# Kernel tuning notes

Hardware: AMD Instinct MI355X
Metric: run time of the kernel (lower is better)

## Reference

```python
import jax, jax.numpy as jnp
import numpy as np
from jax import lax

BN_EPS = 1e-5
DIST_EPS = 1e-8

def _three_nn_interpolate(xyz1, xyz2, points2):
    # squared pairwise distances: (B, N, S)
    d2 = (jnp.sum(xyz1 ** 2, -1)[:, :, None]
          + jnp.sum(xyz2 ** 2, -1)[:, None, :]
          - 2.0 * jnp.einsum('bnd,bsd->bns', xyz1, xyz2))
    neg_d, idx = lax.top_k(-d2, 3)            # 3 nearest -> (B, N, 3)
    dist = -neg_d
    recip = 1.0 / (dist + DIST_EPS)
    weight = recip / jnp.sum(recip, -1, keepdims=True)   # (B, N, 3)
    gathered = jax.vmap(lambda p, i: p[i])(points2, idx)  # (B, N, 3, C2)
    return jnp.einsum('bnkc,bnk->bnc', gathered, weight)

def _conv_bn_relu(x, w, g, b):
    # x: (B, N, Cin); 1x1 conv == matmul; BatchNorm1d over (B, N) per channel (training stats)
    y = jnp.einsum('bnc,oc->bno', x, w)
    mu = jnp.mean(y, axis=(0, 1))
    var = jnp.mean((y - mu) ** 2, axis=(0, 1))
    yn = (y - mu) * lax.rsqrt(var + BN_EPS)
    return jax.nn.relu(yn * g + b)

def setup_inputs() -> dict:
    key = jax.random.key(0)
    ks = jax.random.split(key, 6)
    B, N, S, C1, C2 = 16, 4096, 1024, 256, 256
    return {
        'xyz1': jax.random.normal(ks[0], (B, N, 3), jnp.float32),
        'xyz2': jax.random.normal(ks[1], (B, S, 3), jnp.float32),
        'points1': jax.random.normal(ks[2], (B, N, C1), jnp.float32),
        'points2': jax.random.normal(ks[3], (B, S, C2), jnp.float32),
        'w1': jax.random.normal(ks[4], (256, C1 + C2), jnp.float32) * 0.04,
        'g1': jnp.ones((256,), jnp.float32),
        'b1': jnp.zeros((256,), jnp.float32),
        'w2': jax.random.normal(ks[5], (256, 256), jnp.float32) * 0.06,
        'g2': jnp.ones((256,), jnp.float32),
        'b2': jnp.zeros((256,), jnp.float32),
    }

def reference(xyz1, xyz2, points1, points2, w1, g1, b1, w2, g2, b2):
    interp = _three_nn_interpolate(xyz1, xyz2, points2)    # (B, N, C2)
    feats = jnp.concatenate([points1, interp], axis=-1)    # (B, N, C1+C2)
    h = _conv_bn_relu(feats, w1, g1, b1)
    out = _conv_bn_relu(h, w2, g2, b2)
    return out                                              # (B, N, 256)
```

## Files before the change

### kernel.cpp

```cpp
#include <hip/hip_runtime.h>
#include <stdint.h>

typedef unsigned short ushort_t;
typedef __bf16 bf16x8 __attribute__((ext_vector_type(8)));
typedef float f32x4 __attribute__((ext_vector_type(4)));
typedef unsigned short ushort8 __attribute__((ext_vector_type(8)));
typedef unsigned short ushort4_t __attribute__((ext_vector_type(4)));

#define DEV static __device__ __forceinline__

DEV unsigned short f2bf(float f) {
    union { float f; unsigned int i; } v; v.f = f;
    unsigned int u = v.i;
    return (unsigned short)((u + 0x7fffu + ((u >> 16) & 1u)) >> 16);
}
DEV float bf2f(unsigned short u) {
    union { unsigned int i; float f; } v; v.i = ((unsigned int)u) << 16; return v.f;
}
DEV bf16x8 u2b(ushort8 u) { union { ushort8 u; bf16x8 b; } x; x.u = u; return x.b; }

__global__ __launch_bounds__(256) void cvt_kernel(
    const float* __restrict__ in, ushort_t* __restrict__ out, int n)
{
    int i = blockIdx.x * 256 + threadIdx.x;
    if (i < n) out[i] = f2bf(in[i]);
}

__global__ __launch_bounds__(256) void cvt4_kernel(
    const float* __restrict__ in, ushort_t* __restrict__ out)
{
    int i = (blockIdx.x * 256 + threadIdx.x) * 4;
    float4 v = *(const float4*)(in + i);
    ushort4_t o;
    o[0] = f2bf(v.x); o[1] = f2bf(v.y); o[2] = f2bf(v.z); o[3] = f2bf(v.w);
    *(ushort4_t*)(out + i) = o;
}

__global__ __launch_bounds__(256) void knn_kernel(
    const float* __restrict__ xyz1, const float* __restrict__ xyz2,
    int* __restrict__ idx_out, float* __restrict__ w_out)
{
    __shared__ float4 P[1024];
    __shared__ float mD[24][32];
    __shared__ int   mI[24][32];
    const int b = blockIdx.y;
    const int tid = threadIdx.x;
    for (int s = tid; s < 1024; s += 256) {
        const float* p = xyz2 + ((size_t)b * 1024 + s) * 3;
        float x = p[0], y = p[1], z = p[2];
        float pp = __fadd_rn(__fadd_rn(__fmul_rn(x, x), __fmul_rn(y, y)), __fmul_rn(z, z));
        P[s] = make_float4(x, y, z, pp);
    }
    __syncthreads();
    const int ql = tid & 31;
    const int chunk = tid >> 5;
    const int n = blockIdx.x * 32 + ql;
    const float* q = xyz1 + ((size_t)b * 4096 + n) * 3;
    float qx = q[0], qy = q[1], qz = q[2];
    float qq = __fadd_rn(__fadd_rn(__fmul_rn(qx, qx), __fmul_rn(qy, qy)), __fmul_rn(qz, qz));
    float d0 = 1e30f, d1 = 1e30f, d2 = 1e30f;
    int i0 = 0, i1 = 0, i2 = 0;
    const int s0 = chunk * 128;
#pragma unroll 4
    for (int s = s0; s < s0 + 128; ++s) {
        float4 p = P[s];
        float dot = __fadd_rn(__fadd_rn(__fmul_rn(qx, p.x), __fmul_rn(qy, p.y)), __fmul_rn(qz, p.z));
        float d = __fsub_rn(__fadd_rn(qq, p.w), __fmul_rn(2.0f, dot));
        if (d < d2) {
            if (d < d1) {
                d2 = d1; i2 = i1;
                if (d < d0) { d1 = d0; i1 = i0; d0 = d; i0 = s; }
                else        { d1 = d;  i1 = s; }
            } else { d2 = d; i2 = s; }
        }
    }
    mD[chunk * 3 + 0][ql] = d0; mI[chunk * 3 + 0][ql] = i0;
    mD[chunk * 3 + 1][ql] = d1; mI[chunk * 3 + 1][ql] = i1;
    mD[chunk * 3 + 2][ql] = d2; mI[chunk * 3 + 2][ql] = i2;
    __syncthreads();
    if (tid < 32) {
        float e0 = 1e30f, e1 = 1e30f, e2 = 1e30f;
        int j0 = 0, j1 = 0, j2 = 0;
#pragma unroll
        for (int c = 0; c < 24; ++c) {
            float d = mD[c][ql]; int i = mI[c][ql];
            if (d < e2) {
                if (d < e1) {
                    e2 = e1; j2 = j1;
                    if (d < e0) { e1 = e0; j1 = j0; e0 = d; j0 = i; }
                    else        { e1 = d;  j1 = i; }
                } else { e2 = d; j2 = i; }
            }
        }
        float r0 = 1.0f / (e0 + 1e-8f);
        float r1 = 1.0f / (e1 + 1e-8f);
        float r2 = 1.0f / (e2 + 1e-8f);
        float rs = __fadd_rn(__fadd_rn(r0, r1), r2);
        size_t o = ((size_t)b * 4096 + n) * 3;
        idx_out[o + 0] = j0; idx_out[o + 1] = j1; idx_out[o + 2] = j2;
        w_out[o + 0] = r0 / rs; w_out[o + 1] = r1 / rs; w_out[o + 2] = r2 / rs;
    }
}

__global__ __launch_bounds__(256) void interp_kernel(
    const ushort_t* __restrict__ p2b, const int* __restrict__ idx,
    const float* __restrict__ wgt, ushort_t* __restrict__ itp)
{
    const int t = blockIdx.x * 256 + threadIdx.x;
    const int q = t >> 3;
    const int cg = (t & 7) * 32;
    const size_t o = (size_t)q * 3;
    int i0 = idx[o], i1 = idx[o + 1], i2 = idx[o + 2];
    float w0 = wgt[o], w1 = wgt[o + 1], w2 = wgt[o + 2];
    const ushort_t* pb = p2b + (size_t)(q >> 12) * (1024 * 256);
    const ushort8* g0 = (const ushort8*)(pb + (size_t)i0 * 256 + cg);
    const ushort8* g1 = (const ushort8*)(pb + (size_t)i1 * 256 + cg);
    const ushort8* g2 = (const ushort8*)(pb + (size_t)i2 * 256 + cg);
    ushort8* dst = (ushort8*)(itp + (size_t)q * 256 + cg);
#pragma unroll
    for (int s = 0; s < 4; ++s) {
        ushort8 a = g0[s], b = g1[s], c = g2[s];
        ushort8 ov;
#pragma unroll
        for (int j = 0; j < 8; ++j) {
            float acc = __fmul_rn(w0, bf2f(a[j]));
            acc = fmaf(w1, bf2f(b[j]), acc);
            acc = fmaf(w2, bf2f(c[j]), acc);
            ov[j] = f2bf(acc);
        }
        dst[s] = ov;
    }
}

DEV void cvt8(const float4& u0, const float4& u1, ushort8& hv) {
    hv[0] = f2bf(u0.x); hv[1] = f2bf(u0.y); hv[2] = f2bf(u0.z); hv[3] = f2bf(u0.w);
    hv[4] = f2bf(u1.x); hv[5] = f2bf(u1.y); hv[6] = f2bf(u1.z); hv[7] = f2bf(u1.w);
}

__global__ __launch_bounds__(1024, 4) void gemm1_kernel(
    const float* __restrict__ p1, const ushort_t* __restrict__ itp,
    const ushort_t* __restrict__ w1b, ushort_t* __restrict__ y,
    float* __restrict__ sums, float* __restrict__ sqs)
{
    __shared__ __align__(16) char smem[133120];
    ushort_t* Bs = (ushort_t*)smem;
    const int tid = threadIdx.x;
    const int wave = tid >> 6, lane = tid & 63;
    const int frl = lane & 15, fq = lane >> 4;
    const int panel = blockIdx.x >> 1, nb = blockIdx.x & 1;
    const int m0 = panel * 256;

    {
        const int c = tid >> 3, qq = tid & 7;
        const ushort_t* src = w1b + (size_t)(nb * 128 + c) * 512;
        ushort_t* dst = Bs + c * 520;
#pragma unroll
        for (int s = 0; s < 8; ++s) {
            int off = qq * 8 + s * 64;
            *(ushort8*)(dst + off) = *(const ushort8*)(src + off);
        }
    }

    f32x4 acc[8];
#pragma unroll
    for (int j = 0; j < 8; ++j) acc[j] = f32x4{0.0f, 0.0f, 0.0f, 0.0f};

    __syncthreads();

    const int row0 = m0 + wave * 16 + frl;
    bf16x8 afb[2], bfb[2][8];

#define G1_LOADA(buf, kc) {                                                        \
    if ((kc) < 8) {                                                                \
        const float4* g = (const float4*)(p1 + (size_t)row0 * 256                  \
                                          + (kc) * 32 + fq * 8);                   \
        float4 u0 = g[0], u1 = g[1];                                               \
        ushort8 hv; cvt8(u0, u1, hv);                                              \
        buf = u2b(hv);                                                             \
    } else {                                                                       \
        buf = *(const bf16x8*)(itp + (size_t)row0 * 256                            \
                               + ((kc) - 8) * 32 + fq * 8);                        \
    } }
#define G1_LOADB(buf, kc) { _Pragma("unroll")                                      \
    for (int j = 0; j < 8; ++j)                                                    \
        buf[j] = *(const bf16x8*)(Bs + (j * 16 + frl) * 520 + (kc) * 32 + fq * 8); }

    G1_LOADA(afb[0], 0); G1_LOADB(bfb[0], 0);
#pragma unroll
    for (int kc = 0; kc < 16; ++kc) {
        const int cur = kc & 1, nxt = cur ^ 1;
        if (kc < 15) { G1_LOADA(afb[nxt], kc + 1); G1_LOADB(bfb[nxt], kc + 1); }
#pragma unroll
        for (int j = 0; j < 8; ++j)
            acc[j] = __builtin_amdgcn_mfma_f32_16x16x32_bf16(afb[cur], bfb[cur][j], acc[j], 0, 0, 0);
    }

    float ps[8], pq[8];
#pragma unroll
    for (int j = 0; j < 8; ++j) {
        const int colg = nb * 128 + j * 16 + frl;
        float s = 0.f, q = 0.f;
#pragma unroll
        for (int rr = 0; rr < 4; ++rr) {
            ushort_t hb = f2bf(acc[j][rr]);
            float v = bf2f(hb);
            y[(size_t)(m0 + wave * 16 + fq * 4 + rr) * 256 + colg] = hb;
            s += v; q = fmaf(v, v, q);
        }
        s += __shfl_xor(s, 16); s += __shfl_xor(s, 32);
        q += __shfl_xor(q, 16); q += __shfl_xor(q, 32);
        ps[j] = s; pq[j] = q;
    }
    __syncthreads();
    float* scrS = (float*)smem;
    float* scrQ = (float*)(smem + 8192);
    if (fq == 0) {
#pragma unroll
        for (int j = 0; j < 8; ++j) {
            scrS[wave * 128 + j * 16 + frl] = ps[j];
            scrQ[wave * 128 + j * 16 + frl] = pq[j];
        }
    }
    __syncthreads();
    if (tid < 128) {
        float s = 0.f, q = 0.f;
#pragma unroll
        for (int w = 0; w < 16; ++w) { s += scrS[w * 128 + tid]; q += scrQ[w * 128 + tid]; }
        atomicAdd(&sums[nb * 128 + tid], s);
        atomicAdd(&sqs[nb * 128 + tid], q);
    }
}

__global__ __launch_bounds__(512, 2) void gemm2_kernel(
    const ushort_t* __restrict__ y1, const ushort_t* __restrict__ w2b,
    const float* __restrict__ a1, const float* __restrict__ c1,
    ushort_t* __restrict__ y2, float* __restrict__ sums, float* __restrict__ sqs)
{
    __shared__ __align__(16) char smem[137216];
    ushort_t* As = (ushort_t*)smem;
    ushort_t* Bs = (ushort_t*)(smem + 67584);
    float* sAv = (float*)(smem + 135168);
    float* sCv = (float*)(smem + 136192);
    const int tid = threadIdx.x;
    const int wave = tid >> 6, lane = tid & 63;
    const int frl = lane & 15, fq = lane >> 4;
    const int panel = blockIdx.x >> 1, nb = blockIdx.x & 1;
    const int m0 = panel * 128;

    if (tid < 256) { sAv[tid] = a1[tid]; sCv[tid] = c1[tid]; }
    __syncthreads();

    {
        const int r = tid >> 2, qq = tid & 3;
        const ushort_t* srcA = y1 + (size_t)(m0 + r) * 256;
        ushort_t* dstA = As + r * 264;
        const ushort_t* srcB = w2b + (size_t)(nb * 128 + r) * 256;
        ushort_t* dstB = Bs + r * 264;
#pragma unroll
        for (int s = 0; s < 8; ++s) {
            int off = qq * 8 + s * 32;
            ushort8 raw = *(const ushort8*)(srcA + off);
            ushort8 hv;
#pragma unroll
            for (int e = 0; e < 8; ++e) {
                float v = bf2f(raw[e]);
                hv[e] = f2bf(fmaxf(fmaf(v, sAv[off + e], sCv[off + e]), 0.0f));
            }
            *(ushort8*)(dstA + off) = hv;
            *(ushort8*)(dstB + off) = *(const ushort8*)(srcB + off);
        }
    }

    f32x4 acc[2][4];
#pragma unroll
    for (int i = 0; i < 2; ++i)
#pragma unroll
        for (int j = 0; j < 4; ++j) acc[i][j] = f32x4{0.0f, 0.0f, 0.0f, 0.0f};

    __syncthreads();

    const int rg = (wave & 3) * 32, cg = (wave >> 2) * 64;
    bf16x8 afb[2][2], bfb[2][4];

#define G2_LOADA(buf, kc) { _Pragma("unroll")                                      \
    for (int i = 0; i < 2; ++i)                                                    \
        buf[i] = *(const bf16x8*)(As + (rg + i * 16 + frl) * 264 + (kc) * 32 + fq * 8); }
#define G2_LOADB(buf, kc) { _Pragma("unroll")                                      \
    for (int j = 0; j < 4; ++j)                                                    \
        buf[j] = *(const bf16x8*)(Bs + (cg + j * 16 + frl) * 264 + (kc) * 32 + fq * 8); }

    G2_LOADA(afb[0], 0); G2_LOADB(bfb[0], 0);
#pragma unroll
    for (int kc = 0; kc < 8; ++kc) {
        const int cur = kc & 1, nxt = cur ^ 1;
        if (kc < 7) { G2_LOADA(afb[nxt], kc + 1); G2_LOADB(bfb[nxt], kc + 1); }
#pragma unroll
        for (int i = 0; i < 2; ++i)
#pragma unroll
            for (int j = 0; j < 4; ++j)
                acc[i][j] = __builtin_amdgcn_mfma_f32_16x16x32_bf16(afb[cur][i], bfb[cur][j], acc[i][j], 0, 0, 0);
    }

    float ps[4], pq[4];
#pragma unroll
    for (int j = 0; j < 4; ++j) {
        const int colg = nb * 128 + cg + j * 16 + frl;
        float s = 0.f, q = 0.f;
#pragma unroll
        for (int i = 0; i < 2; ++i)
#pragma unroll
            for (int rr = 0; rr < 4; ++rr) {
                ushort_t hb = f2bf(acc[i][j][rr]);
                float v = bf2f(hb);
                y2[(size_t)(m0 + rg + i * 16 + fq * 4 + rr) * 256 + colg] = hb;
                s += v; q = fmaf(v, v, q);
            }
        s += __shfl_xor(s, 16); s += __shfl_xor(s, 32);
        q += __shfl_xor(q, 16); q += __shfl_xor(q, 32);
        ps[j] = s; pq[j] = q;
    }
    __syncthreads();
    float* scrS = (float*)smem;
    float* scrQ = (float*)(smem + 2048);
    if (fq == 0) {
#pragma unroll
        for (int j = 0; j < 4; ++j) {
            scrS[wave * 64 + j * 16 + frl] = ps[j];
            scrQ[wave * 64 + j * 16 + frl] = pq[j];
        }
    }
    __syncthreads();
    if (tid < 128) {
        const int g = tid >> 6, cw = tid & 63;
        float s = 0.f, q = 0.f;
#pragma unroll
        for (int k = 0; k < 4; ++k) {
            s += scrS[(g * 4 + k) * 64 + cw];
            q += scrQ[(g * 4 + k) * 64 + cw];
        }
        atomicAdd(&sums[nb * 128 + g * 64 + cw], s);
        atomicAdd(&sqs[nb * 128 + g * 64 + cw], q);
    }
}

__global__ __launch_bounds__(256) void finalize_kernel(
    const float* __restrict__ sums, const float* __restrict__ sqs,
    const float* __restrict__ g, const float* __restrict__ bias,
    float* __restrict__ a, float* __restrict__ c)
{
    const int ch = threadIdx.x;
    const float inv_n = 1.0f / 65536.0f;
    float mu = sums[ch] * inv_n;
    float var = fmaf(-mu, mu, sqs[ch] * inv_n);
    float is = 1.0f / sqrtf(var + 1e-5f);
    float aa = g[ch] * is;
    a[ch] = aa;
    c[ch] = fmaf(-mu, aa, bias[ch]);
}

__global__ __launch_bounds__(256) void apply_kernel(
    const ushort_t* __restrict__ y2, const float* __restrict__ a,
    const float* __restrict__ c, float* __restrict__ out)
{
    const size_t i = ((size_t)blockIdx.x * 256 + threadIdx.x) * 8;
    const int ch = (int)(i & 255);
    ushort8 raw = *(const ushort8*)(y2 + i);
    float4 o0, o1;
    const float4 a0 = *(const float4*)(a + ch), a1v = *(const float4*)(a + ch + 4);
    const float4 c0 = *(const float4*)(c + ch), c1v = *(const float4*)(c + ch + 4);
    o0.x = fmaxf(fmaf(bf2f(raw[0]), a0.x, c0.x), 0.0f);
    o0.y = fmaxf(fmaf(bf2f(raw[1]), a0.y, c0.y), 0.0f);
    o0.z = fmaxf(fmaf(bf2f(raw[2]), a0.z, c0.z), 0.0f);
    o0.w = fmaxf(fmaf(bf2f(raw[3]), a0.w, c0.w), 0.0f);
    o1.x = fmaxf(fmaf(bf2f(raw[4]), a1v.x, c1v.x), 0.0f);
    o1.y = fmaxf(fmaf(bf2f(raw[5]), a1v.y, c1v.y), 0.0f);
    o1.z = fmaxf(fmaf(bf2f(raw[6]), a1v.z, c1v.z), 0.0f);
    o1.w = fmaxf(fmaf(bf2f(raw[7]), a1v.w, c1v.w), 0.0f);
    *(float4*)(out + i) = o0;
    *(float4*)(out + i + 4) = o1;
}

extern "C" void kernel_launch(void* const* d_in, const int* in_sizes, int n_in,
                              void* d_out, int out_size, void* d_ws, size_t ws_size,
                              hipStream_t stream)
{
    const float* xyz1    = (const float*)d_in[0];
    const float* xyz2    = (const float*)d_in[1];
    const float* points1 = (const float*)d_in[2];
    const float* points2 = (const float*)d_in[3];
    const float* w1      = (const float*)d_in[4];
    const float* g1      = (const float*)d_in[5];
    const float* b1      = (const float*)d_in[6];
    const float* w2      = (const float*)d_in[7];
    const float* g2      = (const float*)d_in[8];
    const float* b2      = (const float*)d_in[9];
    float* out = (float*)d_out;

    char* ws = (char*)d_ws;
    float* sums1 = (float*)(ws + 0);
    float* sqs1  = (float*)(ws + 1024);
    float* a1    = (float*)(ws + 2048);
    float* c1    = (float*)(ws + 3072);
    float* sums2 = (float*)(ws + 4096);
    float* sqs2  = (float*)(ws + 5120);
    float* a2    = (float*)(ws + 6144);
    float* c2    = (float*)(ws + 7168);
    ushort_t* w1b = (ushort_t*)(ws + (64u << 10));
    ushort_t* w2b = (ushort_t*)(ws + (320u << 10));
    ushort_t* p2b = (ushort_t*)(ws + (1u << 20));
    int*   idx   = (int*)(ws + (10u << 20));
    float* wgt   = (float*)(ws + (11u << 20));
    ushort_t* itp = (ushort_t*)(ws + (12u << 20));
    ushort_t* y1  = (ushort_t*)(ws + (44u << 20));
    ushort_t* y2b = itp;

    hipMemsetAsync(ws, 0, 8192, stream);
    cvt_kernel<<<dim3(512), 256, 0, stream>>>(w1, w1b, 131072);
    cvt_kernel<<<dim3(256), 256, 0, stream>>>(w2, w2b, 65536);
    cvt4_kernel<<<dim3(4096), 256, 0, stream>>>(points2, p2b);
    knn_kernel<<<dim3(128, 16), 256, 0, stream>>>(xyz1, xyz2, idx, wgt);
    interp_kernel<<<dim3(2048), 256, 0, stream>>>(p2b, idx, wgt, itp);
    gemm1_kernel<<<dim3(512), 1024, 0, stream>>>(points1, itp, w1b, y1, sums1, sqs1);
    finalize_kernel<<<dim3(1), 256, 0, stream>>>(sums1, sqs1, g1, b1, a1, c1);
    gemm2_kernel<<<dim3(1024), 512, 0, stream>>>(y1, w2b, a1, c1, y2b, sums2, sqs2);
    finalize_kernel<<<dim3(1), 256, 0, stream>>>(sums2, sqs2, g2, b2, a2, c2);
    apply_kernel<<<dim3(8192), 256, 0, stream>>>(y2b, a2, c2, out);
}
```

Measured before the change: 285.1 us.

## Fuse interpolation into GEMM1, merge prep kernels, fold BN finalize into consumers

Removes the separate interpolation kernel: GEMM1 now gathers the three neighbour rows of bf16 points2 and blends them while loading its A operand. This avoids writing and re-reading the 32MB interpolated buffer. The three conversion kernels and the stats memset are merged into one prep kernel, and each BN finalize is recomputed per block inside gemm2 and apply, which cuts five launches. The cost is uncoalesced gather loads in GEMM1's inner loop and redundant per-block finalize math.

```diff
diff --git a/kernel.cpp b/kernel.cpp
--- a/kernel.cpp
+++ b/kernel.cpp
@@ -19,21 +19,30 @@
 }
 DEV bf16x8 u2b(ushort8 u) { union { ushort8 u; bf16x8 b; } x; x.u = u; return x.b; }
 
-__global__ __launch_bounds__(256) void cvt_kernel(
-    const float* __restrict__ in, ushort_t* __restrict__ out, int n)
-{
-    int i = blockIdx.x * 256 + threadIdx.x;
-    if (i < n) out[i] = f2bf(in[i]);
-}
-
-__global__ __launch_bounds__(256) void cvt4_kernel(
-    const float* __restrict__ in, ushort_t* __restrict__ out)
-{
-    int i = (blockIdx.x * 256 + threadIdx.x) * 4;
-    float4 v = *(const float4*)(in + i);
-    ushort4_t o;
-    o[0] = f2bf(v.x); o[1] = f2bf(v.y); o[2] = f2bf(v.z); o[3] = f2bf(v.w);
-    *(ushort4_t*)(out + i) = o;
+__global__ __launch_bounds__(256) void prep_kernel(
+    const float* __restrict__ w1, const float* __restrict__ w2,
+    const float* __restrict__ points2,
+    ushort_t* __restrict__ w1b, ushort_t* __restrict__ w2b,
+    ushort_t* __restrict__ p2b, float* __restrict__ stats)
+{
+    const int bx = blockIdx.x;
+    if (bx < 512) {
+        int i = bx * 256 + threadIdx.x;
+        w1b[i] = f2bf(w1[i]);
+    } else if (bx < 768) {
+        int i = (bx - 512) * 256 + threadIdx.x;
+        w2b[i] = f2bf(w2[i]);
+    } else if (bx < 4864) {
+        int i = ((bx - 768) * 256 + threadIdx.x) * 4;
+        float4 v = *(const float4*)(points2 + i);
+        ushort4_t o;
+        o[0] = f2bf(v.x); o[1] = f2bf(v.y); o[2] = f2bf(v.z); o[3] = f2bf(v.w);
+        *(ushort4_t*)(p2b + i) = o;
+    } else {
+        int i = threadIdx.x * 8;
+        *(float4*)(stats + i)     = make_float4(0.f, 0.f, 0.f, 0.f);
+        *(float4*)(stats + i + 4) = make_float4(0.f, 0.f, 0.f, 0.f);
+    }
 }
 
 __global__ __launch_bounds__(256) void knn_kernel(
@@ -102,43 +111,14 @@
     }
 }
 
-__global__ __launch_bounds__(256) void interp_kernel(
-    const ushort_t* __restrict__ p2b, const int* __restrict__ idx,
-    const float* __restrict__ wgt, ushort_t* __restrict__ itp)
-{
-    const int t = blockIdx.x * 256 + threadIdx.x;
-    const int q = t >> 3;
-    const int cg = (t & 7) * 32;
-    const size_t o = (size_t)q * 3;
-    int i0 = idx[o], i1 = idx[o + 1], i2 = idx[o + 2];
-    float w0 = wgt[o], w1 = wgt[o + 1], w2 = wgt[o + 2];
-    const ushort_t* pb = p2b + (size_t)(q >> 12) * (1024 * 256);
-    const ushort8* g0 = (const ushort8*)(pb + (size_t)i0 * 256 + cg);
-    const ushort8* g1 = (const ushort8*)(pb + (size_t)i1 * 256 + cg);
-    const ushort8* g2 = (const ushort8*)(pb + (size_t)i2 * 256 + cg);
-    ushort8* dst = (ushort8*)(itp + (size_t)q * 256 + cg);
-#pragma unroll
-    for (int s = 0; s < 4; ++s) {
-        ushort8 a = g0[s], b = g1[s], c = g2[s];
-        ushort8 ov;
-#pragma unroll
-        for (int j = 0; j < 8; ++j) {
-            float acc = __fmul_rn(w0, bf2f(a[j]));
-            acc = fmaf(w1, bf2f(b[j]), acc);
-            acc = fmaf(w2, bf2f(c[j]), acc);
-            ov[j] = f2bf(acc);
-        }
-        dst[s] = ov;
-    }
-}
-
 DEV void cvt8(const float4& u0, const float4& u1, ushort8& hv) {
     hv[0] = f2bf(u0.x); hv[1] = f2bf(u0.y); hv[2] = f2bf(u0.z); hv[3] = f2bf(u0.w);
     hv[4] = f2bf(u1.x); hv[5] = f2bf(u1.y); hv[6] = f2bf(u1.z); hv[7] = f2bf(u1.w);
 }
 
 __global__ __launch_bounds__(1024, 4) void gemm1_kernel(
-    const float* __restrict__ p1, const ushort_t* __restrict__ itp,
+    const float* __restrict__ p1, const ushort_t* __restrict__ p2b,
+    const int* __restrict__ idx, const float* __restrict__ wgt,
     const ushort_t* __restrict__ w1b, ushort_t* __restrict__ y,
     float* __restrict__ sums, float* __restrict__ sqs)
 {
@@ -165,9 +145,16 @@
 #pragma unroll
     for (int j = 0; j < 8; ++j) acc[j] = f32x4{0.0f, 0.0f, 0.0f, 0.0f};
 
-    __syncthreads();
-
     const int row0 = m0 + wave * 16 + frl;
+    const size_t io = (size_t)row0 * 3;
+    const float iw0 = wgt[io], iw1 = wgt[io + 1], iw2 = wgt[io + 2];
+    const ushort_t* pb = p2b + (size_t)(row0 >> 12) * (1024 * 256);
+    const ushort_t* gp0 = pb + (size_t)idx[io] * 256 + fq * 8;
+    const ushort_t* gp1 = pb + (size_t)idx[io + 1] * 256 + fq * 8;
+    const ushort_t* gp2 = pb + (size_t)idx[io + 2] * 256 + fq * 8;
+
+    __syncthreads();
+
     bf16x8 afb[2], bfb[2][8];
 
 #define G1_LOADA(buf, kc) {                                                        \
@@ -178,8 +165,18 @@
         ushort8 hv; cvt8(u0, u1, hv);                                              \
         buf = u2b(hv);                                                             \
     } else {                                                                       \
-        buf = *(const bf16x8*)(itp + (size_t)row0 * 256                            \
-                               + ((kc) - 8) * 32 + fq * 8);                        \
+        ushort8 ga = *(const ushort8*)(gp0 + ((kc) - 8) * 32);                     \
+        ushort8 gb = *(const ushort8*)(gp1 + ((kc) - 8) * 32);                     \
+        ushort8 gc = *(const ushort8*)(gp2 + ((kc) - 8) * 32);                     \
+        ushort8 hv;                                                                \
+        _Pragma("unroll")                                                          \
+        for (int e = 0; e < 8; ++e) {                                              \
+            float av = __fmul_rn(iw0, bf2f(ga[e]));                                \
+            av = fmaf(iw1, bf2f(gb[e]), av);                                       \
+            av = fmaf(iw2, bf2f(gc[e]), av);                                       \
+            hv[e] = f2bf(av);                                                      \
+        }                                                                          \
+        buf = u2b(hv);                                                             \
     } }
 #define G1_LOADB(buf, kc) { _Pragma("unroll")                                      \
     for (int j = 0; j < 8; ++j)                                                    \
@@ -233,7 +230,8 @@
 
 __global__ __launch_bounds__(512, 2) void gemm2_kernel(
     const ushort_t* __restrict__ y1, const ushort_t* __restrict__ w2b,
-    const float* __restrict__ a1, const float* __restrict__ c1,
+    const float* __restrict__ sums1, const float* __restrict__ sqs1,
+    const float* __restrict__ g1, const float* __restrict__ b1,
     ushort_t* __restrict__ y2, float* __restrict__ sums, float* __restrict__ sqs)
 {
     __shared__ __align__(16) char smem[137216];
@@ -247,7 +245,15 @@
     const int panel = blockIdx.x >> 1, nb = blockIdx.x & 1;
     const int m0 = panel * 128;
 
-    if (tid < 256) { sAv[tid] = a1[tid]; sCv[tid] = c1[tid]; }
+    if (tid < 256) {
+        const float inv_n = 1.0f / 65536.0f;
+        float mu = sums1[tid] * inv_n;
+        float var = fmaf(-mu, mu, sqs1[tid] * inv_n);
+        float is = 1.0f / sqrtf(var + 1e-5f);
+        float aa = g1[tid] * is;
+        sAv[tid] = aa;
+        sCv[tid] = fmaf(-mu, aa, b1[tid]);
+    }
     __syncthreads();
 
     {
@@ -343,31 +349,30 @@
     }
 }
 
-__global__ __launch_bounds__(256) void finalize_kernel(
-    const float* __restrict__ sums, const float* __restrict__ sqs,
-    const float* __restrict__ g, const float* __restrict__ bias,
-    float* __restrict__ a, float* __restrict__ c)
-{
-    const int ch = threadIdx.x;
-    const float inv_n = 1.0f / 65536.0f;
-    float mu = sums[ch] * inv_n;
-    float var = fmaf(-mu, mu, sqs[ch] * inv_n);
-    float is = 1.0f / sqrtf(var + 1e-5f);
-    float aa = g[ch] * is;
-    a[ch] = aa;
-    c[ch] = fmaf(-mu, aa, bias[ch]);
-}
-
 __global__ __launch_bounds__(256) void apply_kernel(
-    const ushort_t* __restrict__ y2, const float* __restrict__ a,
-    const float* __restrict__ c, float* __restrict__ out)
-{
+    const ushort_t* __restrict__ y2,
+    const float* __restrict__ sums2, const float* __restrict__ sqs2,
+    const float* __restrict__ g2, const float* __restrict__ b2,
+    float* __restrict__ out)
+{
+    __shared__ float sA[256], sC[256];
+    {
+        const int ch2 = threadIdx.x;
+        const float inv_n = 1.0f / 65536.0f;
+        float mu = sums2[ch2] * inv_n;
+        float var = fmaf(-mu, mu, sqs2[ch2] * inv_n);
+        float is = 1.0f / sqrtf(var + 1e-5f);
+        float aa = g2[ch2] * is;
+        sA[ch2] = aa;
+        sC[ch2] = fmaf(-mu, aa, b2[ch2]);
+    }
+    __syncthreads();
     const size_t i = ((size_t)blockIdx.x * 256 + threadIdx.x) * 8;
     const int ch = (int)(i & 255);
     ushort8 raw = *(const ushort8*)(y2 + i);
     float4 o0, o1;
-    const float4 a0 = *(const float4*)(a + ch), a1v = *(const float4*)(a + ch + 4);
-    const float4 c0 = *(const float4*)(c + ch), c1v = *(const float4*)(c + ch + 4);
+    const float4 a0 = *(const float4*)(sA + ch), a1v = *(const float4*)(sA + ch + 4);
+    const float4 c0 = *(const float4*)(sC + ch), c1v = *(const float4*)(sC + ch + 4);
     o0.x = fmaxf(fmaf(bf2f(raw[0]), a0.x, c0.x), 0.0f);
     o0.y = fmaxf(fmaf(bf2f(raw[1]), a0.y, c0.y), 0.0f);
     o0.z = fmaxf(fmaf(bf2f(raw[2]), a0.z, c0.z), 0.0f);
@@ -399,30 +404,19 @@
     char* ws = (char*)d_ws;
     float* sums1 = (float*)(ws + 0);
     float* sqs1  = (float*)(ws + 1024);
-    float* a1    = (float*)(ws + 2048);
-    float* c1    = (float*)(ws + 3072);
     float* sums2 = (float*)(ws + 4096);
     float* sqs2  = (float*)(ws + 5120);
-    float* a2    = (float*)(ws + 6144);
-    float* c2    = (float*)(ws + 7168);
     ushort_t* w1b = (ushort_t*)(ws + (64u << 10));
     ushort_t* w2b = (ushort_t*)(ws + (320u << 10));
     ushort_t* p2b = (ushort_t*)(ws + (1u << 20));
     int*   idx   = (int*)(ws + (10u << 20));
     float* wgt   = (float*)(ws + (11u << 20));
-    ushort_t* itp = (ushort_t*)(ws + (12u << 20));
+    ushort_t* y2b = (ushort_t*)(ws + (12u << 20));
     ushort_t* y1  = (ushort_t*)(ws + (44u << 20));
-    ushort_t* y2b = itp;
-
-    hipMemsetAsync(ws, 0, 8192, stream);
-    cvt_kernel<<<dim3(512), 256, 0, stream>>>(w1, w1b, 131072);
-    cvt_kernel<<<dim3(256), 256, 0, stream>>>(w2, w2b, 65536);
-    cvt4_kernel<<<dim3(4096), 256, 0, stream>>>(points2, p2b);
+
+    prep_kernel<<<dim3(4865), 256, 0, stream>>>(w1, w2, points2, w1b, w2b, p2b, (float*)ws);
     knn_kernel<<<dim3(128, 16), 256, 0, stream>>>(xyz1, xyz2, idx, wgt);
-    interp_kernel<<<dim3(2048), 256, 0, stream>>>(p2b, idx, wgt, itp);
-    gemm1_kernel<<<dim3(512), 1024, 0, stream>>>(points1, itp, w1b, y1, sums1, sqs1);
-    finalize_kernel<<<dim3(1), 256, 0, stream>>>(sums1, sqs1, g1, b1, a1, c1);
-    gemm2_kernel<<<dim3(1024), 512, 0, stream>>>(y1, w2b, a1, c1, y2b, sums2, sqs2);
-    finalize_kernel<<<dim3(1), 256, 0, stream>>>(sums2, sqs2, g2, b2, a2, c2);
-    apply_kernel<<<dim3(8192), 256, 0, stream>>>(y2b, a2, c2, out);
-}
+    gemm1_kernel<<<dim3(512), 1024, 0, stream>>>(points1, p2b, idx, wgt, w1b, y1, sums1, sqs1);
+    gemm2_kernel<<<dim3(1024), 512, 0, stream>>>(y1, w2b, sums1, sqs1, g1, b1, y2b, sums2, sqs2);
+    apply_kernel<<<dim3(8192), 256, 0, stream>>>(y2b, sums2, sqs2, g2, b2, out);
+}
```

Measured after the change: 275.8 us. 1.03x faster.
